# Optimization experiments

Measured on AMD Instinct MI355X. Metric: run time of the kernel, lower is better.

Reference implementation:

```python
import jax, jax.numpy as jnp
import numpy as np

N = 50000   # nodes
E = 800000  # edges (avg degree 16)
D = 128     # input feature dim
H = 128     # hidden_units per FFN layer
BN_EPS = 1e-3  # keras BatchNormalization default epsilon


def setup_inputs() -> dict:
    key = jax.random.key(0)
    ks = jax.random.split(key, 16)
    inp = {}
    inp["node_repr"] = jax.random.normal(ks[0], (N, D), dtype=jnp.float32)
    inp["edges"] = jax.random.randint(ks[1], (2, E), 0, N, dtype=jnp.int32)
    inp["edge_weights"] = jnp.ones((E,), jnp.float32)
    idx = 2
    # ffn_prepare: D -> H -> H ; update_fn: (D+H) -> H -> H
    for pre, dims in [("prep", [(D, H), (H, H)]), ("upd", [(D + H, H), (H, H)])]:
        for li, (din, dout) in enumerate(dims):
            inp[f"{pre}_bn{li}_g"] = jnp.ones((din,), jnp.float32)
            inp[f"{pre}_bn{li}_b"] = jnp.zeros((din,), jnp.float32)
            inp[f"{pre}_bn{li}_m"] = jax.random.normal(ks[idx], (din,), dtype=jnp.float32) * 0.1; idx += 1
            inp[f"{pre}_bn{li}_v"] = jnp.ones((din,), jnp.float32)
            inp[f"{pre}_W{li}"] = jax.random.normal(ks[idx], (din, dout), dtype=jnp.float32) * (din ** -0.5); idx += 1
            inp[f"{pre}_b{li}"] = jnp.zeros((dout,), jnp.float32)
    return inp


def _ffn(x, layers):
    # layers: list of (bn_gamma, bn_beta, bn_mean, bn_var, W, b)
    # each block: BatchNorm (inference) -> Dropout (identity at eval) -> Dense+gelu
    for g, b, m, v, W, bias in layers:
        x = (x - m) * jax.lax.rsqrt(v + BN_EPS) * g + b
        x = jax.nn.gelu(x @ W + bias, approximate=False)
    return x


def reference(node_repr, edges, edge_weights,
              prep_bn0_g, prep_bn0_b, prep_bn0_m, prep_bn0_v, prep_W0, prep_b0,
              prep_bn1_g, prep_bn1_b, prep_bn1_m, prep_bn1_v, prep_W1, prep_b1,
              upd_bn0_g, upd_bn0_b, upd_bn0_m, upd_bn0_v, upd_W0, upd_b0,
              upd_bn1_g, upd_bn1_b, upd_bn1_m, upd_bn1_v, upd_W1, upd_b1):
    node_indices, neighbour_indices = edges[0], edges[1]
    # prepare: gather neighbours, per-edge FFN, scale by edge weight
    nbr = jnp.take(node_repr, neighbour_indices, axis=0)  # [E, D]
    prep_layers = [(prep_bn0_g, prep_bn0_b, prep_bn0_m, prep_bn0_v, prep_W0, prep_b0),
                   (prep_bn1_g, prep_bn1_b, prep_bn1_m, prep_bn1_v, prep_W1, prep_b1)]
    messages = _ffn(nbr, prep_layers) * edge_weights[:, None]  # [E, H]
    # aggregate: unsorted_segment_mean (empty segments -> 0, as in TF)
    ssum = jax.ops.segment_sum(messages, node_indices, num_segments=node_repr.shape[0])
    cnt = jax.ops.segment_sum(jnp.ones((messages.shape[0],), messages.dtype), node_indices,
                              num_segments=node_repr.shape[0])
    agg = jnp.where(cnt[:, None] > 0, ssum / jnp.maximum(cnt, 1.0)[:, None], 0.0)  # [N, H]
    # update: concat + FFN
    h = jnp.concatenate([node_repr, agg], axis=1)  # [N, D+H]
    upd_layers = [(upd_bn0_g, upd_bn0_b, upd_bn0_m, upd_bn0_v, upd_W0, upd_b0),
                  (upd_bn1_g, upd_bn1_b, upd_bn1_m, upd_bn1_v, upd_W1, upd_b1)]
    return _ffn(h, upd_layers)  # [N, H]
```

## Files before the change

kernel.cpp:

```cpp
#include <hip/hip_runtime.h>
#include <math.h>

#define NN 50000
#define NE 800000
#define DD 128
#define HH 128
#define BN_EPS 1e-3f
#define PBLK 1563
#define EBLK 3125
#define WBLK 512
#define PGRID 512
#define MAXD 64

typedef _Float16 f16x8 __attribute__((ext_vector_type(8)));
typedef float f32x4 __attribute__((ext_vector_type(4)));

#define PIN(v) asm volatile("" : : "v"(v))

__device__ __forceinline__ float gelu_f(float x) {
    float t = x * (1.5957691f + 0.07135481f * x * x);
    float e = __expf(-t);
    return x * __builtin_amdgcn_rcpf(1.0f + e);
}

struct WArgs {
    const float *W, *g, *bb, *m, *v, *bias;
    _Float16* wt; float* bs; int K;
};

__global__ __launch_bounds__(256)
void wdeg_kernel(WArgs a0, WArgs a1, WArgs a2, WArgs a3,
                 const int* __restrict__ edges, int* __restrict__ deg,
                 int* __restrict__ pos)
{
    if (blockIdx.x >= WBLK) {
        int e = (blockIdx.x - WBLK) * 256 + threadIdx.x;
        if (e < NE) pos[e] = atomicAdd(&deg[edges[e]], 1);
        return;
    }
    __shared__ float red[256];
    const int which = blockIdx.x >> 7;
    const int n = blockIdx.x & 127;
    WArgs a = a0;
    if (which == 1) a = a1;
    else if (which == 2) a = a2;
    else if (which == 3) a = a3;
    const int t = threadIdx.x;
    float part = 0.0f;
    for (int k = t; k < a.K; k += 256) {
        float sc = a.g[k] * rsqrtf(a.v[k] + BN_EPS);
        float sh = a.bb[k] - a.m[k] * sc;
        float wv = a.W[(long long)k * HH + n];
        a.wt[(long long)n * a.K + k] = (_Float16)(wv * sc);
        part += sh * wv;
    }
    red[t] = part;
    __syncthreads();
    for (int s = 128; s > 0; s >>= 1) {
        if (t < s) red[t] += red[t + s];
        __syncthreads();
    }
    if (t == 0) a.bs[n] = a.bias[n] + red[0];
}

__global__ __launch_bounds__(256, 2)
void prep_fill_kernel(const float* __restrict__ x,
                      const _Float16* __restrict__ wt0, const float* __restrict__ bs0,
                      const _Float16* __restrict__ wt1, const float* __restrict__ bs1,
                      _Float16* __restrict__ msg,
                      const int* __restrict__ edges, const float* __restrict__ ew,
                      const int* __restrict__ pos, unsigned* __restrict__ rec)
{
    __shared__ __align__(16) _Float16 ys[32 * HH];
    if (blockIdx.x >= PGRID) {
        int e = (blockIdx.x - PGRID) * 256 + threadIdx.x;
        if (e < NE) {
            int d = edges[e];
            int p = pos[e];
            if (p < MAXD) {
                _Float16 hw = (_Float16)ew[e];
                unsigned short hb = __builtin_bit_cast(unsigned short, hw);
                unsigned r = (unsigned)edges[NE + e] | ((unsigned)hb << 16);
                rec[(long long)d * MAXD + p] = r;
            }
        }
        return;
    }
    const int tid = threadIdx.x;
    const int w = tid >> 6, lane = tid & 63;
    const int cl = lane & 15;
    const int kg = lane >> 4;

    f16x8 b0[4][2], b1[4][2];
#pragma unroll
    for (int kc = 0; kc < 4; ++kc)
#pragma unroll
        for (int ct = 0; ct < 2; ++ct) {
            int col = w * 32 + ct * 16 + cl;
            b0[kc][ct] = *reinterpret_cast<const f16x8*>(&wt0[(long long)col * DD + kc * 32 + kg * 8]);
            b1[kc][ct] = *reinterpret_cast<const f16x8*>(&wt1[(long long)col * HH + kc * 32 + kg * 8]);
        }
#pragma unroll
    for (int kc = 0; kc < 4; ++kc) { PIN(b0[kc][0]); PIN(b0[kc][1]); PIN(b1[kc][0]); PIN(b1[kc][1]); }

    const f32x4 zero = {0.0f, 0.0f, 0.0f, 0.0f};

    for (int tile = blockIdx.x; tile < PBLK; tile += PGRID) {
        const int row0 = tile * 32;

        f32x4 acc[2][2];
#pragma unroll
        for (int rt = 0; rt < 2; ++rt)
#pragma unroll
            for (int ct = 0; ct < 2; ++ct) acc[rt][ct] = zero;

#pragma unroll
        for (int kc = 0; kc < 4; ++kc) {
#pragma unroll
            for (int rt = 0; rt < 2; ++rt) {
                int row = row0 + rt * 16 + cl;
                if (row >= NN) row = NN - 1;
                const float4* p = reinterpret_cast<const float4*>(&x[(long long)row * DD + kc * 32 + kg * 8]);
                float4 u0 = p[0], u1 = p[1];
                f16x8 a;
                a[0] = (_Float16)u0.x; a[1] = (_Float16)u0.y; a[2] = (_Float16)u0.z; a[3] = (_Float16)u0.w;
                a[4] = (_Float16)u1.x; a[5] = (_Float16)u1.y; a[6] = (_Float16)u1.z; a[7] = (_Float16)u1.w;
#pragma unroll
                for (int ct = 0; ct < 2; ++ct)
                    acc[rt][ct] = __builtin_amdgcn_mfma_f32_16x16x32_f16(a, b0[kc][ct], acc[rt][ct], 0, 0, 0);
            }
        }

#pragma unroll
        for (int ct = 0; ct < 2; ++ct) {
            int col = w * 32 + ct * 16 + cl;
            float bias = bs0[col];
#pragma unroll
            for (int rt = 0; rt < 2; ++rt)
#pragma unroll
                for (int rr = 0; rr < 4; ++rr) {
                    int r = rt * 16 + kg * 4 + rr;
                    float vv = gelu_f(acc[rt][ct][rr] + bias);
                    int slot = (r * 16 + (col >> 3)) ^ (r & 7);
                    ys[slot * 8 + (col & 7)] = (_Float16)vv;
                }
        }
        __syncthreads();

        f32x4 acc2[2][2];
#pragma unroll
        for (int rt = 0; rt < 2; ++rt)
#pragma unroll
            for (int ct = 0; ct < 2; ++ct) acc2[rt][ct] = zero;

#pragma unroll
        for (int kc = 0; kc < 4; ++kc) {
            int k8 = kc * 4 + kg;
#pragma unroll
            for (int rt = 0; rt < 2; ++rt) {
                int rA = rt * 16 + cl;
                int slot = (rA * 16 + k8) ^ (rA & 7);
                f16x8 a = *reinterpret_cast<const f16x8*>(&ys[slot * 8]);
#pragma unroll
                for (int ct = 0; ct < 2; ++ct)
                    acc2[rt][ct] = __builtin_amdgcn_mfma_f32_16x16x32_f16(a, b1[kc][ct], acc2[rt][ct], 0, 0, 0);
            }
        }

#pragma unroll
        for (int ct = 0; ct < 2; ++ct) {
            int col = w * 32 + ct * 16 + cl;
            float bias = bs1[col];
#pragma unroll
            for (int rt = 0; rt < 2; ++rt)
#pragma unroll
                for (int rr = 0; rr < 4; ++rr) {
                    int row = row0 + rt * 16 + kg * 4 + rr;
                    if (row < NN)
                        msg[(long long)row * HH + col] = (_Float16)gelu_f(acc2[rt][ct][rr] + bias);
                }
        }
        __syncthreads();
    }
}

__global__ __launch_bounds__(256)
void gather_kernel(const int* __restrict__ deg, const unsigned* __restrict__ rec,
                   const _Float16* __restrict__ msg, _Float16* __restrict__ aggh)
{
    int gwave = (blockIdx.x * 256 + threadIdx.x) >> 6;
    int lane = threadIdx.x & 63;
    int sub = lane >> 4, l16 = lane & 15;
    int node = gwave * 4 + sub;
    if (node >= NN) return;
    int dfull = deg[node];
    int d = (dfull > MAXD) ? MAXD : dfull;
    long long beg = (long long)node * MAXD;
    float acc[8];
#pragma unroll
    for (int q = 0; q < 8; ++q) acc[q] = 0.0f;

    for (int base = 0; base < d; base += 16) {
        int nb = d - base;
        if (nb > 16) nb = 16;
        int idx = base + ((l16 < nb) ? l16 : 0);
        unsigned rc = rec[beg + idx];
        for (int j = 0; j < nb; ++j) {
            unsigned r = (unsigned)__shfl((int)rc, sub * 16 + j, 64);
            int src = (int)(r & 0xFFFFu);
            _Float16 hw = __builtin_bit_cast(_Float16, (unsigned short)(r >> 16));
            float wv = (float)hw;
            f16x8 m = *reinterpret_cast<const f16x8*>(&msg[(long long)src * HH + l16 * 8]);
#pragma unroll
            for (int q = 0; q < 8; ++q) acc[q] += (float)m[q] * wv;
        }
    }

    float inv = (dfull > 0) ? 1.0f / (float)dfull : 0.0f;
    f16x8 o;
#pragma unroll
    for (int q = 0; q < 8; ++q) o[q] = (_Float16)(acc[q] * inv);
    *reinterpret_cast<f16x8*>(&aggh[(long long)node * HH + l16 * 8]) = o;
}

__global__ __launch_bounds__(256, 2)
void upd_kernel(const float* __restrict__ x, const _Float16* __restrict__ aggh,
                const _Float16* __restrict__ wt2, const float* __restrict__ bs2,
                const _Float16* __restrict__ wt3, const float* __restrict__ bs3,
                float* __restrict__ out)
{
    __shared__ __align__(16) _Float16 ys[32 * HH];
    const int tid = threadIdx.x;
    const int w = tid >> 6, lane = tid & 63;
    const int cl = lane & 15;
    const int kg = lane >> 4;

    f16x8 b0[8][2], b1[4][2];
#pragma unroll
    for (int kc = 0; kc < 8; ++kc)
#pragma unroll
        for (int ct = 0; ct < 2; ++ct) {
            int col = w * 32 + ct * 16 + cl;
            b0[kc][ct] = *reinterpret_cast<const f16x8*>(&wt2[(long long)col * 256 + kc * 32 + kg * 8]);
        }
#pragma unroll
    for (int kc = 0; kc < 4; ++kc)
#pragma unroll
        for (int ct = 0; ct < 2; ++ct) {
            int col = w * 32 + ct * 16 + cl;
            b1[kc][ct] = *reinterpret_cast<const f16x8*>(&wt3[(long long)col * HH + kc * 32 + kg * 8]);
        }
#pragma unroll
    for (int kc = 0; kc < 4; ++kc) { PIN(b0[kc][0]); PIN(b0[kc][1]); PIN(b1[kc][0]); PIN(b1[kc][1]); }
#pragma unroll
    for (int kc = 4; kc < 8; ++kc) { PIN(b0[kc][0]); PIN(b0[kc][1]); }

    const f32x4 zero = {0.0f, 0.0f, 0.0f, 0.0f};

    for (int tile = blockIdx.x; tile < PBLK; tile += PGRID) {
        const int row0 = tile * 32;

        f32x4 acc[2][2];
#pragma unroll
        for (int rt = 0; rt < 2; ++rt)
#pragma unroll
            for (int ct = 0; ct < 2; ++ct) acc[rt][ct] = zero;

#pragma unroll
        for (int kc = 0; kc < 8; ++kc) {
#pragma unroll
            for (int rt = 0; rt < 2; ++rt) {
                int row = row0 + rt * 16 + cl;
                if (row >= NN) row = NN - 1;
                f16x8 a;
                if (kc < 4) {
                    const float4* p = reinterpret_cast<const float4*>(&x[(long long)row * DD + kc * 32 + kg * 8]);
                    float4 u0 = p[0], u1 = p[1];
                    a[0] = (_Float16)u0.x; a[1] = (_Float16)u0.y; a[2] = (_Float16)u0.z; a[3] = (_Float16)u0.w;
                    a[4] = (_Float16)u1.x; a[5] = (_Float16)u1.y; a[6] = (_Float16)u1.z; a[7] = (_Float16)u1.w;
                } else {
                    a = *reinterpret_cast<const f16x8*>(&aggh[(long long)row * HH + (kc - 4) * 32 + kg * 8]);
                }
#pragma unroll
                for (int ct = 0; ct < 2; ++ct)
                    acc[rt][ct] = __builtin_amdgcn_mfma_f32_16x16x32_f16(a, b0[kc][ct], acc[rt][ct], 0, 0, 0);
            }
        }

#pragma unroll
        for (int ct = 0; ct < 2; ++ct) {
            int col = w * 32 + ct * 16 + cl;
            float bias = bs2[col];
#pragma unroll
            for (int rt = 0; rt < 2; ++rt)
#pragma unroll
                for (int rr = 0; rr < 4; ++rr) {
                    int r = rt * 16 + kg * 4 + rr;
                    float vv = gelu_f(acc[rt][ct][rr] + bias);
                    int slot = (r * 16 + (col >> 3)) ^ (r & 7);
                    ys[slot * 8 + (col & 7)] = (_Float16)vv;
                }
        }
        __syncthreads();

        f32x4 acc2[2][2];
#pragma unroll
        for (int rt = 0; rt < 2; ++rt)
#pragma unroll
            for (int ct = 0; ct < 2; ++ct) acc2[rt][ct] = zero;

#pragma unroll
        for (int kc = 0; kc < 4; ++kc) {
            int k8 = kc * 4 + kg;
#pragma unroll
            for (int rt = 0; rt < 2; ++rt) {
                int rA = rt * 16 + cl;
                int slot = (rA * 16 + k8) ^ (rA & 7);
                f16x8 a = *reinterpret_cast<const f16x8*>(&ys[slot * 8]);
#pragma unroll
                for (int ct = 0; ct < 2; ++ct)
                    acc2[rt][ct] = __builtin_amdgcn_mfma_f32_16x16x32_f16(a, b1[kc][ct], acc2[rt][ct], 0, 0, 0);
            }
        }

#pragma unroll
        for (int ct = 0; ct < 2; ++ct) {
            int col = w * 32 + ct * 16 + cl;
            float bias = bs3[col];
#pragma unroll
            for (int rt = 0; rt < 2; ++rt)
#pragma unroll
                for (int rr = 0; rr < 4; ++rr) {
                    int row = row0 + rt * 16 + kg * 4 + rr;
                    if (row < NN)
                        out[(long long)row * HH + col] = gelu_f(acc2[rt][ct][rr] + bias);
                }
        }
        __syncthreads();
    }
}

extern "C" void kernel_launch(void* const* d_in, const int* in_sizes, int n_in,
                              void* d_out, int out_size, void* d_ws, size_t ws_size,
                              hipStream_t stream) {
    const float* node_repr = (const float*)d_in[0];
    const int*   edges     = (const int*)d_in[1];
    const float* ew        = (const float*)d_in[2];

    const float* prep_bn0_g = (const float*)d_in[3];
    const float* prep_bn0_b = (const float*)d_in[4];
    const float* prep_bn0_m = (const float*)d_in[5];
    const float* prep_bn0_v = (const float*)d_in[6];
    const float* prep_W0    = (const float*)d_in[7];
    const float* prep_b0    = (const float*)d_in[8];
    const float* prep_bn1_g = (const float*)d_in[9];
    const float* prep_bn1_b = (const float*)d_in[10];
    const float* prep_bn1_m = (const float*)d_in[11];
    const float* prep_bn1_v = (const float*)d_in[12];
    const float* prep_W1    = (const float*)d_in[13];
    const float* prep_b1    = (const float*)d_in[14];

    const float* upd_bn0_g = (const float*)d_in[15];
    const float* upd_bn0_b = (const float*)d_in[16];
    const float* upd_bn0_m = (const float*)d_in[17];
    const float* upd_bn0_v = (const float*)d_in[18];
    const float* upd_W0    = (const float*)d_in[19];
    const float* upd_b0    = (const float*)d_in[20];
    const float* upd_bn1_g = (const float*)d_in[21];
    const float* upd_bn1_b = (const float*)d_in[22];
    const float* upd_bn1_m = (const float*)d_in[23];
    const float* upd_bn1_v = (const float*)d_in[24];
    const float* upd_W1    = (const float*)d_in[25];
    const float* upd_b1    = (const float*)d_in[26];

    _Float16* msg  = (_Float16*)d_ws;
    _Float16* aggh = msg + (size_t)NN * HH;
    _Float16* wt0  = aggh + (size_t)NN * HH;
    _Float16* wt1  = wt0 + 128 * 128;
    _Float16* wt2  = wt1 + 128 * 128;
    _Float16* wt3  = wt2 + 128 * 256;
    float* bs0 = (float*)(wt3 + 128 * 128);
    float* bs1 = bs0 + 128;
    float* bs2 = bs1 + 128;
    float* bs3 = bs2 + 128;
    int* deg    = (int*)(bs3 + 128);
    int* pos    = deg + NN;
    unsigned* rec = (unsigned*)(pos + NE);

    hipMemsetAsync(deg, 0, (size_t)NN * sizeof(int), stream);

    WArgs a0 = {prep_W0, prep_bn0_g, prep_bn0_b, prep_bn0_m, prep_bn0_v, prep_b0, wt0, bs0, DD};
    WArgs a1 = {prep_W1, prep_bn1_g, prep_bn1_b, prep_bn1_m, prep_bn1_v, prep_b1, wt1, bs1, HH};
    WArgs a2 = {upd_W0, upd_bn0_g, upd_bn0_b, upd_bn0_m, upd_bn0_v, upd_b0, wt2, bs2, DD + HH};
    WArgs a3 = {upd_W1, upd_bn1_g, upd_bn1_b, upd_bn1_m, upd_bn1_v, upd_b1, wt3, bs3, HH};

    wdeg_kernel<<<WBLK + EBLK, 256, 0, stream>>>(a0, a1, a2, a3, edges, deg, pos);

    prep_fill_kernel<<<PGRID + EBLK, 256, 0, stream>>>(node_repr, wt0, bs0, wt1, bs1,
                                                       msg, edges, ew, pos, rec);

    int gblk = (NN + 15) / 16;
    gather_kernel<<<gblk, 256, 0, stream>>>(deg, rec, msg, aggh);

    upd_kernel<<<PGRID, 256, 0, stream>>>(node_repr, aggh, wt2, bs2, wt3, bs3,
                                          (float*)d_out);
}
```

Before: 141.5 us.

## Fuse neighbour gather-mean into the update FFN kernel via shared memory

The separate gather kernel is removed. Each update tile now gathers and averages the messages for its 32 nodes directly into a swizzled shared-memory buffer, which feeds the first MFMA layer in place of reading the global aggregate array. This drops one kernel launch and the write and re-read of an N x H fp16 intermediate. In exchange the irregular gather now runs inside a kernel with a 512-block grid and two blocks per CU, so it has less parallelism to hide latency, and there is no overlap between the gather and the matrix work.

```diff
diff --git a/kernel.cpp b/kernel.cpp
--- a/kernel.cpp
+++ b/kernel.cpp
@@ -184,56 +184,21 @@
     }
 }
 
-__global__ __launch_bounds__(256)
-void gather_kernel(const int* __restrict__ deg, const unsigned* __restrict__ rec,
-                   const _Float16* __restrict__ msg, _Float16* __restrict__ aggh)
-{
-    int gwave = (blockIdx.x * 256 + threadIdx.x) >> 6;
-    int lane = threadIdx.x & 63;
-    int sub = lane >> 4, l16 = lane & 15;
-    int node = gwave * 4 + sub;
-    if (node >= NN) return;
-    int dfull = deg[node];
-    int d = (dfull > MAXD) ? MAXD : dfull;
-    long long beg = (long long)node * MAXD;
-    float acc[8];
-#pragma unroll
-    for (int q = 0; q < 8; ++q) acc[q] = 0.0f;
-
-    for (int base = 0; base < d; base += 16) {
-        int nb = d - base;
-        if (nb > 16) nb = 16;
-        int idx = base + ((l16 < nb) ? l16 : 0);
-        unsigned rc = rec[beg + idx];
-        for (int j = 0; j < nb; ++j) {
-            unsigned r = (unsigned)__shfl((int)rc, sub * 16 + j, 64);
-            int src = (int)(r & 0xFFFFu);
-            _Float16 hw = __builtin_bit_cast(_Float16, (unsigned short)(r >> 16));
-            float wv = (float)hw;
-            f16x8 m = *reinterpret_cast<const f16x8*>(&msg[(long long)src * HH + l16 * 8]);
-#pragma unroll
-            for (int q = 0; q < 8; ++q) acc[q] += (float)m[q] * wv;
-        }
-    }
-
-    float inv = (dfull > 0) ? 1.0f / (float)dfull : 0.0f;
-    f16x8 o;
-#pragma unroll
-    for (int q = 0; q < 8; ++q) o[q] = (_Float16)(acc[q] * inv);
-    *reinterpret_cast<f16x8*>(&aggh[(long long)node * HH + l16 * 8]) = o;
-}
-
 __global__ __launch_bounds__(256, 2)
-void upd_kernel(const float* __restrict__ x, const _Float16* __restrict__ aggh,
-                const _Float16* __restrict__ wt2, const float* __restrict__ bs2,
-                const _Float16* __restrict__ wt3, const float* __restrict__ bs3,
-                float* __restrict__ out)
+void gupd_kernel(const float* __restrict__ x,
+                 const int* __restrict__ deg, const unsigned* __restrict__ rec,
+                 const _Float16* __restrict__ msg,
+                 const _Float16* __restrict__ wt2, const float* __restrict__ bs2,
+                 const _Float16* __restrict__ wt3, const float* __restrict__ bs3,
+                 float* __restrict__ out)
 {
     __shared__ __align__(16) _Float16 ys[32 * HH];
+    __shared__ __align__(16) _Float16 ag[32 * HH];
     const int tid = threadIdx.x;
     const int w = tid >> 6, lane = tid & 63;
     const int cl = lane & 15;
     const int kg = lane >> 4;
+    const int sub = lane >> 4, l16 = lane & 15;
 
     f16x8 b0[8][2], b1[4][2];
 #pragma unroll
@@ -259,6 +224,41 @@
 
     for (int tile = blockIdx.x; tile < PBLK; tile += PGRID) {
         const int row0 = tile * 32;
+
+#pragma unroll
+        for (int half = 0; half < 2; ++half) {
+            int r = half * 16 + w * 4 + sub;
+            int node = row0 + r;
+            int dfull = 0;
+            if (node < NN) dfull = deg[node];
+            int d = (dfull > MAXD) ? MAXD : dfull;
+            long long beg = (long long)((node < NN) ? node : 0) * MAXD;
+            float acc[8];
+#pragma unroll
+            for (int q = 0; q < 8; ++q) acc[q] = 0.0f;
+            for (int base = 0; base < d; base += 16) {
+                int nb = d - base;
+                if (nb > 16) nb = 16;
+                int idx = base + ((l16 < nb) ? l16 : 0);
+                unsigned rc = rec[beg + idx];
+                for (int j = 0; j < nb; ++j) {
+                    unsigned rr = (unsigned)__shfl((int)rc, sub * 16 + j, 64);
+                    int src = (int)(rr & 0xFFFFu);
+                    _Float16 hw = __builtin_bit_cast(_Float16, (unsigned short)(rr >> 16));
+                    float wv = (float)hw;
+                    f16x8 m = *reinterpret_cast<const f16x8*>(&msg[(long long)src * HH + l16 * 8]);
+#pragma unroll
+                    for (int q = 0; q < 8; ++q) acc[q] += (float)m[q] * wv;
+                }
+            }
+            float inv = (dfull > 0) ? 1.0f / (float)dfull : 0.0f;
+            f16x8 o;
+#pragma unroll
+            for (int q = 0; q < 8; ++q) o[q] = (_Float16)(acc[q] * inv);
+            int slot = (r * 16 + l16) ^ (r & 7);
+            *reinterpret_cast<f16x8*>(&ag[slot * 8]) = o;
+        }
+        __syncthreads();
 
         f32x4 acc[2][2];
 #pragma unroll
@@ -279,7 +279,9 @@
                     a[0] = (_Float16)u0.x; a[1] = (_Float16)u0.y; a[2] = (_Float16)u0.z; a[3] = (_Float16)u0.w;
                     a[4] = (_Float16)u1.x; a[5] = (_Float16)u1.y; a[6] = (_Float16)u1.z; a[7] = (_Float16)u1.w;
                 } else {
-                    a = *reinterpret_cast<const f16x8*>(&aggh[(long long)row * HH + (kc - 4) * 32 + kg * 8]);
+                    int rA = rt * 16 + cl;
+                    int slot = (rA * 16 + (kc - 4) * 4 + kg) ^ (rA & 7);
+                    a = *reinterpret_cast<const f16x8*>(&ag[slot * 8]);
                 }
 #pragma unroll
                 for (int ct = 0; ct < 2; ++ct)
@@ -374,8 +376,7 @@
     const float* upd_b1    = (const float*)d_in[26];
 
     _Float16* msg  = (_Float16*)d_ws;
-    _Float16* aggh = msg + (size_t)NN * HH;
-    _Float16* wt0  = aggh + (size_t)NN * HH;
+    _Float16* wt0  = msg + (size_t)NN * HH;
     _Float16* wt1  = wt0 + 128 * 128;
     _Float16* wt2  = wt1 + 128 * 128;
     _Float16* wt3  = wt2 + 128 * 256;
@@ -399,9 +400,6 @@
     prep_fill_kernel<<<PGRID + EBLK, 256, 0, stream>>>(node_repr, wt0, bs0, wt1, bs1,
                                                        msg, edges, ew, pos, rec);
 
-    int gblk = (NN + 15) / 16;
-    gather_kernel<<<gblk, 256, 0, stream>>>(deg, rec, msg, aggh);
-
-    upd_kernel<<<PGRID, 256, 0, stream>>>(node_repr, aggh, wt2, bs2, wt3, bs3,
-                                          (float*)d_out);
+    gupd_kernel<<<PGRID, 256, 0, stream>>>(node_repr, deg, rec, msg,
+                                           wt2, bs2, wt3, bs3, (float*)d_out);
 }
```

After: 176.3 us. 1.25x slower.
